# Performance work log

Hardware: AMD Instinct MI355X
Metric: run time of the kernel (lower is better)

## Reference

```python
import jax
import jax.numpy as jnp
import numpy as np
from functools import partial

B, C_CLS, H, W = 1, 2, 480, 854
KS = (7, 7, 9)       # kernel sizes of the 3 pairwise kernels
DILS = (64, 16, 1)   # their dilations
STEPS = 5            # PacCRFLoose: independent params per mean-field step


def unfold2d(x, k, dil):
    """x: [B,C,H,W] -> [B,C,k*k,H,W]: zero-padded dilated k x k neighborhoods."""
    b, c, h, w = x.shape
    pad = (k // 2) * dil
    xp = jnp.pad(x, ((0, 0), (0, 0), (pad, pad), (pad, pad)))
    taps = [xp[:, :, i * dil:i * dil + h, j * dil:j * dil + w]
            for i in range(k) for j in range(k)]
    return jnp.stack(taps, axis=2)


@partial(jax.checkpoint, static_argnums=(1, 2))
def pac_kernel(feat, k, dil):
    """Fixed Gaussian pixel-adaptive kernel exp(-0.5*||f_p - f_q||^2): [B,k*k,H,W]."""
    d = unfold2d(feat, k, dil) - feat[:, :, None]  # center tap diff is 0 -> kernel 1
    return jnp.exp(-0.5 * jnp.sum(d * d, axis=1))


def message(Q, K, k, dil, filt):
    """PacConv2d with shared spatial filter: sum_t w_t * K_t(p) * Q(p + off_t)."""
    Qc = unfold2d(Q, k, dil)  # [B, C, T, H, W]
    return jnp.einsum('bcthw,bthw,t->bchw', Qc, K, filt)


def crf_forward(unary, x, feat_scales, potts_w, unary_weights, pw_weights,
                w_filt0, w_filt1, w_filt2, compat0, compat1):
    b, _, h, w = x.shape
    yy, xx = jnp.meshgrid(jnp.arange(h, dtype=x.dtype),
                          jnp.arange(w, dtype=x.dtype), indexing='ij')
    mesh = jnp.broadcast_to(jnp.stack([yy, xx])[None], (b, 2, h, w))

    # create_YXRGB: channels [y/s0, x/s1, r/s2, g/s3, b/s4]
    feats = [jnp.concatenate([mesh / feat_scales[i, :2, None, None],
                              x / feat_scales[i, 2:, None, None]], axis=1)
             for i in range(3)]
    # create_position_feats appended as 4th edge feature; PacCRF only consumes
    # edge_feat[0..n_kernels-1] so it is dead in the original forward too.
    _pos = mesh * (1.0 / potts_w.reshape(-1, 1, 1))

    # edge kernels are computed once (PacCRFLoose shares them across steps)
    kernels = [pac_kernel(feats[i], KS[i], DILS[i]) for i in range(3)]

    unary5 = unary * 5.0  # ModelWithCrf scales unary by 5 before the CRF

    def step(logQ, p):
        uw, pw, w0, w1, w2, c0, c1 = p
        Q = jax.nn.softmax(logQ, axis=1)
        m0 = jnp.einsum('dc,bchw->bdhw', c0, message(Q, kernels[0], KS[0], DILS[0], w0))
        m1 = jnp.einsum('dc,bchw->bdhw', c1, message(Q, kernels[1], KS[1], DILS[1], w1))
        m2 = message(Q, kernels[2], KS[2], DILS[2], w2)  # potts: no compat conv
        new_logQ = uw * unary5 + pw[0] * m0 + pw[1] * m1 + pw[2] * m2
        return new_logQ, None

    logQ, _ = jax.lax.scan(jax.checkpoint(step), unary5,
                           (unary_weights, pw_weights, w_filt0, w_filt1, w_filt2,
                            compat0, compat1))
    return logQ  # final_output='log_Q'


def setup_inputs():
    key = jax.random.key(0)
    k = jax.random.split(key, 8)
    unary = jax.random.normal(k[0], (B, C_CLS, H, W), jnp.float32)
    x = jax.random.uniform(k[1], (B, 3, H, W), jnp.float32) * 255.0  # RGB frame
    # p_sc = ((5-1)*16+1)/4 = 16.25, c_sc = 30.0 for all 3 scale sets (as in source)
    feat_scales = jnp.tile(jnp.array([16.25, 16.25, 30.0, 30.0, 30.0],
                                     jnp.float32)[None], (3, 1))
    potts_w = jnp.ones((1,), jnp.float32)
    unary_weights = jnp.full((STEPS,), 0.85, jnp.float32)
    pw_weights = jnp.tile(jnp.array([1.0, 1.0, 6.0], jnp.float32)[None], (STEPS, 1))
    pr = 0.001  # perturbed_init range
    w_filt0 = 1.0 / 49 + (jax.random.uniform(k[2], (STEPS, 49)) - 0.5) * pr
    w_filt1 = 1.0 / 49 + (jax.random.uniform(k[3], (STEPS, 49)) - 0.5) * pr
    w_filt2 = 1.0 / 81 + (jax.random.uniform(k[4], (STEPS, 81)) - 0.5) * pr
    off_diag = (1.0 - jnp.eye(C_CLS, dtype=jnp.float32))[None]
    compat0 = off_diag + (jax.random.uniform(k[5], (STEPS, C_CLS, C_CLS)) - 0.5) * pr
    compat1 = off_diag + (jax.random.uniform(k[6], (STEPS, C_CLS, C_CLS)) - 0.5) * pr
    return dict(unary=unary, x=x, feat_scales=feat_scales, potts_w=potts_w,
                unary_weights=unary_weights, pw_weights=pw_weights,
                w_filt0=w_filt0, w_filt1=w_filt1, w_filt2=w_filt2,
                compat0=compat0, compat1=compat1)


def reference(unary, x, feat_scales, potts_w, unary_weights, pw_weights,
              w_filt0, w_filt1, w_filt2, compat0, compat1):
    return crf_forward(unary, x, feat_scales, potts_w, unary_weights, pw_weights,
                       w_filt0, w_filt1, w_filt2, compat0, compat1)
```

## Files before the change

kernel.cpp:

```cpp
#include <hip/hip_runtime.h>

typedef _Float16 h2 __attribute__((ext_vector_type(2)));

#define HH 480
#define WW 854
#define HWSZ (HH * WW)
#define PAD 192
#define PSTR 1240
#define PH (HH + 2 * PAD)
#define PCELLS (PH * PSTR)

#if __has_builtin(__builtin_amdgcn_exp2f)
#define EXP2(x) __builtin_amdgcn_exp2f(x)
#else
#define EXP2(x) exp2f(x)
#endif

__device__ __forceinline__ float fdot2f(h2 a, h2 b, float c)
{
#if __has_builtin(__builtin_amdgcn_fdot2)
    return __builtin_amdgcn_fdot2(a, b, c, false);
#else
    return fmaf((float)a.x, (float)b.x, fmaf((float)a.y, (float)b.y, c));
#endif
}

__device__ __forceinline__ h2 bch2(unsigned u)
{
    union { unsigned u; h2 h; } v; v.u = u; return v.h;
}
__device__ __forceinline__ unsigned h2u(h2 h)
{
    union { h2 h; unsigned u; } v; v.h = h; return v.u;
}
__device__ __forceinline__ float hiq(unsigned u)
{
    union { unsigned u; h2 h; } v; v.u = u; return (float)v.h.y;
}
__device__ __forceinline__ unsigned short hbits(_Float16 h)
{
    union { _Float16 h; unsigned short u; } v; v.h = h; return v.u;
}

__global__ __launch_bounds__(256) void init_P(
    const float* __restrict__ xrgb, const float* __restrict__ fs,
    uint2* __restrict__ PA, uint2* __restrict__ PB)
{
    int i = blockIdx.x * 256 + threadIdx.x;
    if (i >= PCELLS) return;
    int y = i / PSTR, x = i - y * PSTR;
    int iy = y - PAD, ix = x - PAD;
    uint2 v;
    if (iy >= 0 && iy < HH && ix >= 0 && ix < WW) {
        int p = iy * WW + ix;
        _Float16 rh = (_Float16)(xrgb[p] * (1.0f / fs[2]));
        _Float16 gh = (_Float16)(xrgb[HWSZ + p] * (1.0f / fs[3]));
        _Float16 bh = (_Float16)(xrgb[2 * HWSZ + p] * (1.0f / fs[4]));
        v = make_uint2(h2u(h2{rh, gh}), h2u(h2{bh, (_Float16)0}));
    } else {
        v = make_uint2(0x7BFF7BFFu, 0x00007BFFu);
    }
    PA[i] = v;
    PB[i] = v;
}

__global__ __launch_bounds__(256) void pack0(
    const float* __restrict__ unary, unsigned* __restrict__ PAw)
{
    int i = blockIdx.x * 256 + threadIdx.x;
    if (i >= HWSZ) return;
    float l0 = unary[i], l1 = unary[HWSZ + i];
    float q = 1.0f / (1.0f + __expf(5.0f * (l1 - l0)));
    int y = i / WW, x = i - y * WW;
    int c = (y + PAD) * PSTR + x + PAD;
    unsigned old = PAw[2 * c + 1];
    PAw[2 * c + 1] = (old & 0xFFFFu) |
                     ((unsigned)hbits((_Float16)q) << 16);
}

__device__ __forceinline__ void tap8(uint2 aq, h2 rgp, h2 bqp, float nk,
                                     float tpv, float& A, float& B)
{
    h2 drg = bch2(aq.x) - rgp;
    h2 dbq = bch2(aq.y) - bqp;
    h2 dbm = bch2(h2u(dbq) & 0xFFFFu);
    float s1 = fdot2f(drg, drg, 0.0f);
    float ssq = fdot2f(dbm, dbm, s1);
    float e = EXP2(fmaf(ssq, nk, tpv));
    A = fmaf(e, hiq(aq.y), A);
    B += e;
}

template <int K, int D>
__device__ __forceinline__ void row8(const uint2* __restrict__ rp,
                                     const float* __restrict__ tr,
                                     h2 rgp, h2 bqp, float nk,
                                     float& A, float& B)
{
    uint2 buf[K];
#pragma unroll
    for (int j = 0; j < K; ++j) buf[j] = rp[(j - K / 2) * D];
#pragma unroll
    for (int j = 0; j < K; ++j)
        tap8(buf[j], rgp, bqp, nk, tr[j], A, B);
}

template <bool LAST>
__global__ __launch_bounds__(256) void crf_step(
    const uint2* __restrict__ srcP, unsigned* __restrict__ dstPw,
    const float* __restrict__ unary,
    const float* __restrict__ fs, const float* __restrict__ uwArr,
    const float* __restrict__ pwArr,
    const float* __restrict__ w0, const float* __restrict__ w1,
    const float* __restrict__ w2,
    const float* __restrict__ c0, const float* __restrict__ c1,
    int step, float* __restrict__ out)
{
    __shared__ __align__(16) float tp0[7 * 8];
    __shared__ __align__(16) float tp1[7 * 8];
    __shared__ __align__(16) float tp2[9 * 12];
    __shared__ float scal[15];

    const float NH = -0.72134752044448169f;
    int tid = threadIdx.y * 128 + threadIdx.x;

    if (tid < 49) {
        int dy = tid / 7 - 3, dx = tid % 7 - 3;
        float py = dy * 64.0f / fs[0], px = dx * 64.0f / fs[1];
        tp0[(tid / 7) * 8 + tid % 7] =
            log2f(w0[step * 49 + tid]) + NH * (py * py + px * px);
    } else if (tid >= 64 && tid < 113) {
        int t = tid - 64;
        int dy = t / 7 - 3, dx = t % 7 - 3;
        float py = dy * 16.0f / fs[5], px = dx * 16.0f / fs[6];
        tp1[(t / 7) * 8 + t % 7] =
            log2f(w1[step * 49 + t]) + NH * (py * py + px * px);
    } else if (tid >= 128 && tid < 209) {
        int t = tid - 128;
        int dy = t / 9 - 4, dx = t % 9 - 4;
        float py = dy / fs[10], px = dx / fs[11];
        tp2[(t / 9) * 12 + t % 9] =
            log2f(w2[step * 81 + t]) + NH * (py * py + px * px);
    } else if (tid == 224) {
        float r1 = fs[2] / fs[7], r2 = fs[2] / fs[12];
        scal[0] = NH;
        scal[1] = NH * r1 * r1;
        scal[2] = NH * r2 * r2;
        scal[3] = c0[step * 4 + 0];  scal[4] = c0[step * 4 + 1];
        scal[5] = c0[step * 4 + 2];  scal[6] = c0[step * 4 + 3];
        scal[7] = c1[step * 4 + 0];  scal[8] = c1[step * 4 + 1];
        scal[9] = c1[step * 4 + 2];  scal[10] = c1[step * 4 + 3];
        scal[11] = pwArr[step * 3 + 0];
        scal[12] = pwArr[step * 3 + 1];
        scal[13] = pwArr[step * 3 + 2];
        scal[14] = uwArr[step] * 5.0f;
    }
    __syncthreads();

    int x = blockIdx.x * 128 + threadIdx.x;
    int y = blockIdx.y * 2 + threadIdx.y;
    if (x >= WW) return;
    int p = y * WW + x;
    int ccell = (y + PAD) * PSTR + x + PAD;

    float un0 = unary[p], un1 = unary[HWSZ + p];

    const uint2* Pc = srcP + ccell;
    uint2 cw = *Pc;
    h2 rgp = bch2(cw.x);
    h2 bqp = bch2(cw.y);

    float nk0 = scal[0], nk1 = scal[1], nk2 = scal[2];

    float A0 = 0.f, B0 = 0.f, A1 = 0.f, B1 = 0.f, A2 = 0.f, B2 = 0.f;

#pragma unroll
    for (int i = 0; i < 9; ++i) {
        if (i < 7) {
            row8<7, 64>(Pc + (i - 3) * 64 * PSTR, tp0 + i * 8,
                        rgp, bqp, nk0, A0, B0);
            row8<7, 16>(Pc + (i - 3) * 16 * PSTR, tp1 + i * 8,
                        rgp, bqp, nk1, A1, B1);
        }
        row8<9, 1>(Pc + (i - 4) * PSTR, tp2 + i * 12,
                   rgp, bqp, nk2, A2, B2);
    }

    float m00 = A0, m01 = B0 - A0;
    float m10 = A1, m11 = B1 - A1;
    float m20 = A2, m21 = B2 - A2;

    float r00 = scal[3] * m00 + scal[4] * m01;
    float r01 = scal[5] * m00 + scal[6] * m01;
    float r10 = scal[7] * m10 + scal[8] * m11;
    float r11 = scal[9] * m10 + scal[10] * m11;

    float pw0 = scal[11], pw1 = scal[12], pw2 = scal[13], uw5 = scal[14];
    float o0 = uw5 * un0 + pw0 * r00 + pw1 * r10 + pw2 * m20;
    float o1 = uw5 * un1 + pw0 * r01 + pw1 * r11 + pw2 * m21;

    if (LAST) {
        out[p] = o0;
        out[HWSZ + p] = o1;
    } else {
        float qn = 1.0f / (1.0f + __expf(o1 - o0));
        unsigned nb = (h2u(bqp) & 0xFFFFu) |
                      ((unsigned)hbits((_Float16)qn) << 16);
        dstPw[2 * ccell + 1] = nb;
    }
}

extern "C" void kernel_launch(void* const* d_in, const int* in_sizes, int n_in,
                              void* d_out, int out_size, void* d_ws, size_t ws_size,
                              hipStream_t stream)
{
    const float* unary = (const float*)d_in[0];
    const float* xrgb  = (const float*)d_in[1];
    const float* fs    = (const float*)d_in[2];
    const float* uw    = (const float*)d_in[4];
    const float* pw    = (const float*)d_in[5];
    const float* w0    = (const float*)d_in[6];
    const float* w1    = (const float*)d_in[7];
    const float* w2    = (const float*)d_in[8];
    const float* c0    = (const float*)d_in[9];
    const float* c1    = (const float*)d_in[10];
    float* out = (float*)d_out;

    uint2* PA = (uint2*)d_ws;
    uint2* PB = (uint2*)((char*)d_ws + (size_t)PCELLS * 8);

    init_P<<<(PCELLS + 255) / 256, 256, 0, stream>>>(xrgb, fs, PA, PB);
    pack0<<<(HWSZ + 255) / 256, 256, 0, stream>>>(unary, (unsigned*)PA);

    dim3 gs((WW + 127) / 128, HH / 2), bs(128, 2);
    for (int s = 0; s < 5; ++s) {
        const uint2* src = (s & 1) ? PB : PA;
        unsigned* dst = (unsigned*)((s & 1) ? PA : PB);
        if (s < 4)
            crf_step<false><<<gs, bs, 0, stream>>>(src, dst, unary, fs, uw, pw,
                                                   w0, w1, w2, c0, c1, s, out);
        else
            crf_step<true><<<gs, bs, 0, stream>>>(src, dst, unary, fs, uw, pw,
                                                  w0, w1, w2, c0, c1, s, out);
    }
}
```

Before: 195.0 us.

## Stage dilation-16 and dilation-1 neighborhoods in LDS, precompute tap tables

Each block now stages the rows needed by the dilation-16 and dilation-1 kernels into shared memory with wide vector loads, so taps are read from LDS instead of global memory. The per-step tap-weight and scalar tables move into a separate kernel that runs once, which removes the per-block log2 setup and its barrier dependency. The dilation-64 taps stay as global loads, split into batches interleaved with the LDS-based work to overlap latency. Launch bounds now request 3 blocks per CU. The cost is about 36 KB of LDS per block, which may limit occupancy, plus higher register pressure from the load buffers.

```diff
diff --git a/kernel.cpp b/kernel.cpp
--- a/kernel.cpp
+++ b/kernel.cpp
@@ -9,6 +9,7 @@
 #define PSTR 1240
 #define PH (HH + 2 * PAD)
 #define PCELLS (PH * PSTR)
+#define TPSTRIDE 240
 
 #if __has_builtin(__builtin_amdgcn_exp2f)
 #define EXP2(x) __builtin_amdgcn_exp2f(x)
@@ -74,8 +75,53 @@
     int y = i / WW, x = i - y * WW;
     int c = (y + PAD) * PSTR + x + PAD;
     unsigned old = PAw[2 * c + 1];
-    PAw[2 * c + 1] = (old & 0xFFFFu) |
-                     ((unsigned)hbits((_Float16)q) << 16);
+    PAw[2 * c + 1] = (old & 0xFFFFu) | ((unsigned)hbits((_Float16)q) << 16);
+}
+
+__global__ __launch_bounds__(256) void build_tp(
+    const float* __restrict__ fs, const float* __restrict__ uwArr,
+    const float* __restrict__ pwArr,
+    const float* __restrict__ w0, const float* __restrict__ w1,
+    const float* __restrict__ w2,
+    const float* __restrict__ c0, const float* __restrict__ c1,
+    float* __restrict__ tp)
+{
+    int s = blockIdx.x;
+    int t = threadIdx.x;
+    float* d = tp + s * TPSTRIDE;
+    const float NH = -0.72134752044448169f;
+
+    if (t < 49) {
+        int dy = t / 7 - 3, dx = t % 7 - 3;
+        float py = dy * 64.0f / fs[0], px = dx * 64.0f / fs[1];
+        d[(t / 7) * 8 + t % 7] =
+            log2f(w0[s * 49 + t]) + NH * (py * py + px * px);
+    } else if (t >= 64 && t < 113) {
+        int u = t - 64;
+        int dy = u / 7 - 3, dx = u % 7 - 3;
+        float py = dy * 16.0f / fs[5], px = dx * 16.0f / fs[6];
+        d[56 + (u / 7) * 8 + u % 7] =
+            log2f(w1[s * 49 + u]) + NH * (py * py + px * px);
+    } else if (t >= 128 && t < 209) {
+        int u = t - 128;
+        int dy = u / 9 - 4, dx = u % 9 - 4;
+        float py = dy / fs[10], px = dx / fs[11];
+        d[112 + (u / 9) * 12 + u % 9] =
+            log2f(w2[s * 81 + u]) + NH * (py * py + px * px);
+    } else if (t == 224) {
+        float r1 = fs[2] / fs[7], r2 = fs[2] / fs[12];
+        d[220] = NH;
+        d[221] = NH * r1 * r1;
+        d[222] = NH * r2 * r2;
+        d[223] = c0[s * 4 + 0];  d[224] = c0[s * 4 + 1];
+        d[225] = c0[s * 4 + 2];  d[226] = c0[s * 4 + 3];
+        d[227] = c1[s * 4 + 0];  d[228] = c1[s * 4 + 1];
+        d[229] = c1[s * 4 + 2];  d[230] = c1[s * 4 + 3];
+        d[231] = pwArr[s * 3 + 0];
+        d[232] = pwArr[s * 3 + 1];
+        d[233] = pwArr[s * 3 + 2];
+        d[234] = uwArr[s] * 5.0f;
+    }
 }
 
 __device__ __forceinline__ void tap8(uint2 aq, h2 rgp, h2 bqp, float nk,
@@ -91,77 +137,85 @@
     B += e;
 }
 
-template <int K, int D>
-__device__ __forceinline__ void row8(const uint2* __restrict__ rp,
-                                     const float* __restrict__ tr,
-                                     h2 rgp, h2 bqp, float nk,
-                                     float& A, float& B)
-{
-    uint2 buf[K];
-#pragma unroll
-    for (int j = 0; j < K; ++j) buf[j] = rp[(j - K / 2) * D];
-#pragma unroll
-    for (int j = 0; j < K; ++j)
-        tap8(buf[j], rgp, bqp, nk, tr[j], A, B);
+template <int T0, int N>
+__device__ __forceinline__ void loadK0(uint2 (&buf)[N], const uint2* __restrict__ Pc)
+{
+#pragma unroll
+    for (int t = 0; t < N; ++t) {
+        const int tt = T0 + t;
+        buf[t] = Pc[(tt / 7 - 3) * 64 * PSTR + (tt % 7 - 3) * 64];
+    }
+}
+template <int T0, int N>
+__device__ __forceinline__ void compK0(const uint2 (&buf)[N],
+                                       const float* __restrict__ tp0,
+                                       h2 rgp, h2 bqp, float nk,
+                                       float& A, float& B)
+{
+#pragma unroll
+    for (int t = 0; t < N; ++t) {
+        const int tt = T0 + t;
+        tap8(buf[t], rgp, bqp, nk, tp0[(tt / 7) * 8 + tt % 7], A, B);
+    }
+}
+template <int T0, int N>
+__device__ __forceinline__ void compK2(const uint2* __restrict__ T2b,
+                                       const float* __restrict__ tp2,
+                                       h2 rgp, h2 bqp, float nk,
+                                       float& A, float& B)
+{
+#pragma unroll
+    for (int t = 0; t < N; ++t) {
+        const int tt = T0 + t;
+        tap8(T2b[(tt / 9) * 136 + tt % 9], rgp, bqp, nk,
+             tp2[(tt / 9) * 12 + tt % 9], A, B);
+    }
 }
 
 template <bool LAST>
-__global__ __launch_bounds__(256) void crf_step(
+__global__ __launch_bounds__(256, 3) void crf_step(
     const uint2* __restrict__ srcP, unsigned* __restrict__ dstPw,
-    const float* __restrict__ unary,
-    const float* __restrict__ fs, const float* __restrict__ uwArr,
-    const float* __restrict__ pwArr,
-    const float* __restrict__ w0, const float* __restrict__ w1,
-    const float* __restrict__ w2,
-    const float* __restrict__ c0, const float* __restrict__ c1,
+    const float* __restrict__ unary, const float* __restrict__ tpAll,
     int step, float* __restrict__ out)
 {
-    __shared__ __align__(16) float tp0[7 * 8];
-    __shared__ __align__(16) float tp1[7 * 8];
-    __shared__ __align__(16) float tp2[9 * 12];
-    __shared__ float scal[15];
-
-    const float NH = -0.72134752044448169f;
+    __shared__ uint2 T1[14 * 224];
+    __shared__ uint2 T2[10 * 136];
+
     int tid = threadIdx.y * 128 + threadIdx.x;
-
-    if (tid < 49) {
-        int dy = tid / 7 - 3, dx = tid % 7 - 3;
-        float py = dy * 64.0f / fs[0], px = dx * 64.0f / fs[1];
-        tp0[(tid / 7) * 8 + tid % 7] =
-            log2f(w0[step * 49 + tid]) + NH * (py * py + px * px);
-    } else if (tid >= 64 && tid < 113) {
-        int t = tid - 64;
-        int dy = t / 7 - 3, dx = t % 7 - 3;
-        float py = dy * 16.0f / fs[5], px = dx * 16.0f / fs[6];
-        tp1[(t / 7) * 8 + t % 7] =
-            log2f(w1[step * 49 + t]) + NH * (py * py + px * px);
-    } else if (tid >= 128 && tid < 209) {
-        int t = tid - 128;
-        int dy = t / 9 - 4, dx = t % 9 - 4;
-        float py = dy / fs[10], px = dx / fs[11];
-        tp2[(t / 9) * 12 + t % 9] =
-            log2f(w2[step * 81 + t]) + NH * (py * py + px * px);
-    } else if (tid == 224) {
-        float r1 = fs[2] / fs[7], r2 = fs[2] / fs[12];
-        scal[0] = NH;
-        scal[1] = NH * r1 * r1;
-        scal[2] = NH * r2 * r2;
-        scal[3] = c0[step * 4 + 0];  scal[4] = c0[step * 4 + 1];
-        scal[5] = c0[step * 4 + 2];  scal[6] = c0[step * 4 + 3];
-        scal[7] = c1[step * 4 + 0];  scal[8] = c1[step * 4 + 1];
-        scal[9] = c1[step * 4 + 2];  scal[10] = c1[step * 4 + 3];
-        scal[11] = pwArr[step * 3 + 0];
-        scal[12] = pwArr[step * 3 + 1];
-        scal[13] = pwArr[step * 3 + 2];
-        scal[14] = uwArr[step] * 5.0f;
+    int x0 = blockIdx.x * 128, y0 = blockIdx.y * 2;
+
+#pragma unroll
+    for (int r = 0; r < 14; ++r) {
+        if (tid < 112) {
+            int gy = y0 + 16 * (r >> 1) + (r & 1) - 48;
+            const uint4* srow = (const uint4*)
+                (srcP + (gy + PAD) * PSTR + (x0 - 48 + PAD));
+            ((uint4*)T1)[r * 112 + tid] = srow[tid];
+        }
+    }
+#pragma unroll
+    for (int r = 0; r < 10; ++r) {
+        int t2 = tid - 128;
+        if (t2 >= 0 && t2 < 68) {
+            int gy = y0 - 4 + r;
+            const uint4* srow = (const uint4*)
+                (srcP + (gy + PAD) * PSTR + (x0 - 4 + PAD));
+            ((uint4*)T2)[r * 68 + t2] = srow[t2];
+        }
     }
     __syncthreads();
 
-    int x = blockIdx.x * 128 + threadIdx.x;
-    int y = blockIdx.y * 2 + threadIdx.y;
+    int x = x0 + threadIdx.x;
+    int y = y0 + threadIdx.y;
     if (x >= WW) return;
     int p = y * WW + x;
     int ccell = (y + PAD) * PSTR + x + PAD;
+
+    const float* tp0 = tpAll + step * TPSTRIDE;
+    const float* tp1 = tp0 + 56;
+    const float* tp2 = tp0 + 112;
+    const float* sc  = tp0 + 220;
+    float nk0 = sc[0], nk1 = sc[1], nk2 = sc[2];
 
     float un0 = unary[p], un1 = unary[HWSZ + p];
 
@@ -170,32 +224,42 @@
     h2 rgp = bch2(cw.x);
     h2 bqp = bch2(cw.y);
 
-    float nk0 = scal[0], nk1 = scal[1], nk2 = scal[2];
+    const uint2* T1b = T1 + threadIdx.y * 224 + threadIdx.x;
+    const uint2* T2b = T2 + threadIdx.y * 136 + threadIdx.x;
 
     float A0 = 0.f, B0 = 0.f, A1 = 0.f, B1 = 0.f, A2 = 0.f, B2 = 0.f;
 
-#pragma unroll
-    for (int i = 0; i < 9; ++i) {
-        if (i < 7) {
-            row8<7, 64>(Pc + (i - 3) * 64 * PSTR, tp0 + i * 8,
-                        rgp, bqp, nk0, A0, B0);
-            row8<7, 16>(Pc + (i - 3) * 16 * PSTR, tp1 + i * 8,
-                        rgp, bqp, nk1, A1, B1);
-        }
-        row8<9, 1>(Pc + (i - 4) * PSTR, tp2 + i * 12,
-                   rgp, bqp, nk2, A2, B2);
-    }
+    uint2 bA[13], bB[12], bC[12], bD[12];
+    loadK0<0, 13>(bA, Pc);
+    compK2<0, 20>(T2b, tp2, rgp, bqp, nk2, A2, B2);
+    loadK0<13, 12>(bB, Pc);
+    compK0<0, 13>(bA, tp0, rgp, bqp, nk0, A0, B0);
+    compK2<20, 20>(T2b, tp2, rgp, bqp, nk2, A2, B2);
+    loadK0<25, 12>(bC, Pc);
+    compK0<13, 12>(bB, tp0, rgp, bqp, nk0, A0, B0);
+    compK2<40, 20>(T2b, tp2, rgp, bqp, nk2, A2, B2);
+    loadK0<37, 12>(bD, Pc);
+    compK0<25, 12>(bC, tp0, rgp, bqp, nk0, A0, B0);
+    compK2<60, 21>(T2b, tp2, rgp, bqp, nk2, A2, B2);
+    compK0<37, 12>(bD, tp0, rgp, bqp, nk0, A0, B0);
+
+#pragma unroll
+    for (int i = 0; i < 7; ++i)
+#pragma unroll
+        for (int j = 0; j < 7; ++j)
+            tap8(T1b[i * 448 + j * 16], rgp, bqp, nk1,
+                 tp1[i * 8 + j], A1, B1);
 
     float m00 = A0, m01 = B0 - A0;
     float m10 = A1, m11 = B1 - A1;
     float m20 = A2, m21 = B2 - A2;
 
-    float r00 = scal[3] * m00 + scal[4] * m01;
-    float r01 = scal[5] * m00 + scal[6] * m01;
-    float r10 = scal[7] * m10 + scal[8] * m11;
-    float r11 = scal[9] * m10 + scal[10] * m11;
-
-    float pw0 = scal[11], pw1 = scal[12], pw2 = scal[13], uw5 = scal[14];
+    float r00 = sc[3] * m00 + sc[4] * m01;
+    float r01 = sc[5] * m00 + sc[6] * m01;
+    float r10 = sc[7] * m10 + sc[8] * m11;
+    float r11 = sc[9] * m10 + sc[10] * m11;
+
+    float pw0 = sc[11], pw1 = sc[12], pw2 = sc[13], uw5 = sc[14];
     float o0 = uw5 * un0 + pw0 * r00 + pw1 * r10 + pw2 * m20;
     float o1 = uw5 * un1 + pw0 * r01 + pw1 * r11 + pw2 * m21;
 
@@ -228,19 +292,21 @@
 
     uint2* PA = (uint2*)d_ws;
     uint2* PB = (uint2*)((char*)d_ws + (size_t)PCELLS * 8);
+    float* tpAll = (float*)((char*)d_ws + (size_t)PCELLS * 16);
 
     init_P<<<(PCELLS + 255) / 256, 256, 0, stream>>>(xrgb, fs, PA, PB);
     pack0<<<(HWSZ + 255) / 256, 256, 0, stream>>>(unary, (unsigned*)PA);
+    build_tp<<<5, 256, 0, stream>>>(fs, uw, pw, w0, w1, w2, c0, c1, tpAll);
 
     dim3 gs((WW + 127) / 128, HH / 2), bs(128, 2);
     for (int s = 0; s < 5; ++s) {
         const uint2* src = (s & 1) ? PB : PA;
         unsigned* dst = (unsigned*)((s & 1) ? PA : PB);
         if (s < 4)
-            crf_step<false><<<gs, bs, 0, stream>>>(src, dst, unary, fs, uw, pw,
-                                                   w0, w1, w2, c0, c1, s, out);
+            crf_step<false><<<gs, bs, 0, stream>>>(src, dst, unary, tpAll,
+                                                   s, out);
         else
-            crf_step<true><<<gs, bs, 0, stream>>>(src, dst, unary, fs, uw, pw,
-                                                  w0, w1, w2, c0, c1, s, out);
-    }
-}
+            crf_step<true><<<gs, bs, 0, stream>>>(src, dst, unary, tpAll,
+                                                  s, out);
+    }
+}
```

Measured after the change: 185.0 us. 5.1% less time.
